# Kernel optimization log

Measured on AMD Instinct MI355X. Metric: run time of the kernel, lower is better.

## Reference

```python
import jax, jax.numpy as jnp
import numpy as np

B, C, H, W = 8, 256, 48, 48
HW = H * W
DK = C // 8
LN_EPS = 1e-5


def setup_inputs() -> dict:
    key = jax.random.key(0)
    ks = jax.random.split(key, 16)
    s = lambda fan: 1.0 / np.sqrt(fan)
    return {
        "img_feat": jax.random.normal(ks[0], (B, C, H, W), jnp.float32),
        "text_feat": jax.random.normal(ks[1], (B, C), jnp.float32),
        "l": jax.random.normal(ks[2], (1, HW), jnp.float32),
        "Wg1": jax.random.normal(ks[3], (C, 2 * C), jnp.float32) * s(C),
        "bg1": jax.random.normal(ks[4], (2 * C,), jnp.float32) * 0.01,
        "ln_g": jnp.ones((2 * C,), jnp.float32),
        "ln_b": jnp.zeros((2 * C,), jnp.float32),
        "Wg2": jax.random.normal(ks[5], (2 * C, C), jnp.float32) * s(2 * C),
        "bg2": jax.random.normal(ks[6], (C,), jnp.float32) * 0.01,
        "Wq": jax.random.normal(ks[7], (DK, C), jnp.float32) * s(C),
        "bq": jax.random.normal(ks[8], (DK,), jnp.float32) * 0.01,
        "Wk": jax.random.normal(ks[9], (DK, C), jnp.float32) * s(C),
        "bk": jax.random.normal(ks[10], (DK,), jnp.float32) * 0.01,
        "Wv": jax.random.normal(ks[11], (C, C), jnp.float32) * s(C),
        "bv": jax.random.normal(ks[12], (C,), jnp.float32) * 0.01,
        "gamma": jax.random.normal(ks[13], (1,), jnp.float32) * 0.1,
    }


def reference(img_feat, text_feat, l, Wg1, bg1, ln_g, ln_b, Wg2, bg2,
              Wq, bq, Wk, bk, Wv, bv, gamma):
    b, c, h, w = img_feat.shape
    hw = h * w
    # G(text_feat): Linear -> LayerNorm -> GELU (exact) -> Linear
    t = text_feat @ Wg1 + bg1                          # [B, 2C]
    mu = jnp.mean(t, axis=-1, keepdims=True)
    var = jnp.mean((t - mu) ** 2, axis=-1, keepdims=True)
    t = (t - mu) / jnp.sqrt(var + LN_EPS) * ln_g + ln_b
    t = jax.nn.gelu(t, approximate=False)
    GvT = t @ Wg2 + bg2                                # [B, C]
    # F_T = GvT^T outer l  -> [B, C, HW]
    FT = GvT[:, :, None] * l.reshape(-1)[None, None, :]
    x = img_feat.reshape(b, c, hw)
    # 1x1 convs are channel matmuls
    Q = jnp.einsum('dc,bcn->bdn', Wq, x) + bq[None, :, None]   # [B, dk, HW]
    K = jnp.einsum('dc,bcn->bdn', Wk, FT) + bk[None, :, None]  # [B, dk, HW]
    V = jnp.einsum('dc,bcn->bdn', Wv, FT) + bv[None, :, None]  # [B, C, HW]
    # energy = Q^T K (NO 1/sqrt(d_k) scaling, as in the source)
    energy = jnp.einsum('bdi,bdj->bij', Q, K)                  # [B, HW, HW]
    attn = jax.nn.softmax(energy, axis=-1)
    out = jnp.einsum('bcj,bij->bci', V, attn).reshape(b, c, h, w)
    return img_feat + gamma.reshape(()) * out
```

## Files before the change

kernel.cpp:

```cpp
#include <hip/hip_runtime.h>
#include <math.h>

#define B_ 8
#define C_ 256
#define C2_ 512
#define DK_ 32
#define HW_ 2304

#define WS_WQ   0
#define WS_VG   2048
#define WS_QB   4096
#define WS_S    4352

__device__ __forceinline__ float gelu_exact(float x) {
    return 0.5f * x * (1.0f + erff(x * 0.70710678118654752f));
}

__global__ __launch_bounds__(512) void k_prep(
    const float* __restrict__ text,
    const float* __restrict__ Wg1,  const float* __restrict__ bg1,
    const float* __restrict__ ln_g, const float* __restrict__ ln_b,
    const float* __restrict__ Wg2,  const float* __restrict__ bg2,
    const float* __restrict__ Wq,   const float* __restrict__ bq,
    const float* __restrict__ Wk,   const float* __restrict__ Wv,
    float* __restrict__ ws)
{
    const int b = blockIdx.x >> 3;
    const int tile = blockIdx.x & 7;
    const int tid = threadIdx.x;

    __shared__ float tx[C_];
    __shared__ __align__(16) float tsh[C2_];
    __shared__ __align__(16) float gvs[C_];
    __shared__ float part2[2][C_];
    __shared__ float r1[8], r2[8];
    __shared__ float kg[DK_];

    if (tid < C_) tx[tid] = text[b * C_ + tid];
    __syncthreads();

    float acc = bg1[tid];
    #pragma unroll 8
    for (int c = 0; c < C_; ++c)
        acc += tx[c] * Wg1[(size_t)c * C2_ + tid];

    float s1 = acc, s2 = acc * acc;
    for (int o = 32; o; o >>= 1) {
        s1 += __shfl_down(s1, o);
        s2 += __shfl_down(s2, o);
    }
    if ((tid & 63) == 0) { r1[tid >> 6] = s1; r2[tid >> 6] = s2; }
    __syncthreads();
    s1 = 0.f; s2 = 0.f;
    #pragma unroll
    for (int u = 0; u < 8; ++u) { s1 += r1[u]; s2 += r2[u]; }
    const float mu = s1 * (1.0f / 512.0f);
    const float rstd = rsqrtf(s2 * (1.0f / 512.0f) - mu * mu + 1e-5f);
    tsh[tid] = gelu_exact((acc - mu) * rstd * ln_g[tid] + ln_b[tid]);
    __syncthreads();

    {
        const int col = tid & 255, half = tid >> 8;
        float g = 0.f;
        const float* wcol = Wg2 + (size_t)(half * 256) * C_ + col;
        #pragma unroll 8
        for (int j = 0; j < 256; ++j)
            g += tsh[half * 256 + j] * wcol[(size_t)j * C_];
        part2[half][col] = g;
    }
    __syncthreads();
    if (tid < C_) gvs[tid] = part2[0][tid] + part2[1][tid] + bg2[tid];
    __syncthreads();

    const int o = tid >> 4, sub = tid & 15;
    const float4* gv4 = (const float4*)gvs + sub * 4;
    {
        const float4* wrow = (const float4*)(Wv + (size_t)(tile * 32 + o) * C_) + sub * 4;
        float a = 0.f;
        #pragma unroll
        for (int k4 = 0; k4 < 4; ++k4) {
            float4 w4 = wrow[k4], g4 = gv4[k4];
            a += w4.x * g4.x + w4.y * g4.y + w4.z * g4.z + w4.w * g4.w;
        }
        a += __shfl_xor(a, 1);
        a += __shfl_xor(a, 2);
        a += __shfl_xor(a, 4);
        a += __shfl_xor(a, 8);
        if (sub == 0) ws[WS_VG + b * C_ + tile * 32 + o] = a;
    }

    if (tile == 0) {
        const float4* wrow = (const float4*)(Wk + (size_t)o * C_) + sub * 4;
        float a = 0.f;
        #pragma unroll
        for (int k4 = 0; k4 < 4; ++k4) {
            float4 w4 = wrow[k4], g4 = gv4[k4];
            a += w4.x * g4.x + w4.y * g4.y + w4.z * g4.z + w4.w * g4.w;
        }
        a += __shfl_xor(a, 1);
        a += __shfl_xor(a, 2);
        a += __shfl_xor(a, 4);
        a += __shfl_xor(a, 8);
        if (sub == 0) kg[o] = a;
        __syncthreads();
        if (tid < C_) {
            float w = 0.f;
            #pragma unroll
            for (int d = 0; d < DK_; ++d) w += kg[d] * Wq[(size_t)d * C_ + tid];
            ws[WS_WQ + b * C_ + tid] = w;
        }
        if (tid == 0) {
            float q = 0.f;
            #pragma unroll
            for (int d = 0; d < DK_; ++d) q += kg[d] * bq[d];
            ws[WS_QB + b] = q;
        }
    }
}

__global__ __launch_bounds__(256) void k_as(
    const float* __restrict__ img, const float* __restrict__ l,
    float* __restrict__ ws)
{
    const int blk = blockIdx.x;
    const int b = blk / 72;
    const int i0 = (blk % 72) * 32;
    const int tid = threadIdx.x;

    __shared__ float lsh[HW_];
    __shared__ float wq[C_];
    __shared__ float part[8][32];
    __shared__ float aa[32];
    __shared__ float redmn[4], redmx[4];

    wq[tid] = ws[WS_WQ + b * C_ + tid];
    float mn = 1e30f, mx = -1e30f;
    #pragma unroll
    for (int j = tid; j < HW_; j += 256) {
        float v = l[j];
        lsh[j] = v;
        mn = fminf(mn, v); mx = fmaxf(mx, v);
    }
    for (int o = 32; o; o >>= 1) {
        mn = fminf(mn, __shfl_down(mn, o));
        mx = fmaxf(mx, __shfl_down(mx, o));
    }
    if ((tid & 63) == 0) { redmn[tid >> 6] = mn; redmx[tid >> 6] = mx; }
    __syncthreads();
    const float lmin = fminf(fminf(redmn[0], redmn[1]), fminf(redmn[2], redmn[3]));
    const float lmax = fmaxf(fmaxf(redmx[0], redmx[1]), fmaxf(redmx[2], redmx[3]));

    {
        const int pix = tid & 31, sub = tid >> 5;
        const float* x = img + ((size_t)b * C_ + sub * 32) * HW_ + i0 + pix;
        float acc = 0.f;
        #pragma unroll 8
        for (int k = 0; k < 32; ++k)
            acc += wq[sub * 32 + k] * x[(size_t)k * HW_];
        part[sub][pix] = acc;
    }
    __syncthreads();
    if (tid < 32) {
        float a = ws[WS_QB + b];
        #pragma unroll
        for (int u = 0; u < 8; ++u) a += part[u][tid];
        aa[tid] = a;
    }
    __syncthreads();

    const int spix = tid >> 3, ssub = tid & 7;
    const float m = aa[spix];
    const float mxv = (m >= 0.f) ? m * lmax : m * lmin;
    float se = 0.f, sle = 0.f;
    #pragma unroll 4
    for (int j = ssub; j < HW_; j += 8) {
        float lj = lsh[j];
        float e = __expf(m * lj - mxv);
        se += e;
        sle += e * lj;
    }
    se += __shfl_xor(se, 1);  sle += __shfl_xor(sle, 1);
    se += __shfl_xor(se, 2);  sle += __shfl_xor(sle, 2);
    se += __shfl_xor(se, 4);  sle += __shfl_xor(sle, 4);
    if (ssub == 0) ws[WS_S + b * HW_ + i0 + spix] = sle / se;
}

__global__ __launch_bounds__(256) void k_out(
    const float* __restrict__ img, const float* __restrict__ bv,
    const float* __restrict__ gamma, const float* __restrict__ ws,
    float* __restrict__ out)
{
    const float g = gamma[0];
    const size_t idx = (size_t)blockIdx.x * 256 + threadIdx.x;
    const size_t flat = idx * 4;
    const int b = (int)(flat / (C_ * HW_));
    const int rem = (int)(flat % (C_ * HW_));
    const int c = rem / HW_;
    const int i = rem % HW_;

    const float4 im = *(const float4*)(img + flat);
    const float4 s4 = *(const float4*)(ws + WS_S + b * HW_ + i);
    const float vgc = ws[WS_VG + b * C_ + c];
    const float bvc = bv[c];
    float4 o;
    o.x = im.x + g * (vgc * s4.x + bvc);
    o.y = im.y + g * (vgc * s4.y + bvc);
    o.z = im.z + g * (vgc * s4.z + bvc);
    o.w = im.w + g * (vgc * s4.w + bvc);
    *(float4*)(out + flat) = o;
}

extern "C" void kernel_launch(void* const* d_in, const int* in_sizes, int n_in,
                              void* d_out, int out_size, void* d_ws, size_t ws_size,
                              hipStream_t stream) {
    const float* img   = (const float*)d_in[0];
    const float* text  = (const float*)d_in[1];
    const float* l     = (const float*)d_in[2];
    const float* Wg1   = (const float*)d_in[3];
    const float* bg1   = (const float*)d_in[4];
    const float* ln_g  = (const float*)d_in[5];
    const float* ln_b  = (const float*)d_in[6];
    const float* Wg2   = (const float*)d_in[7];
    const float* bg2   = (const float*)d_in[8];
    const float* Wq    = (const float*)d_in[9];
    const float* bq    = (const float*)d_in[10];
    const float* Wk    = (const float*)d_in[11];
    const float* Wv    = (const float*)d_in[13];
    const float* bv    = (const float*)d_in[14];
    const float* gamma = (const float*)d_in[15];
    float* out = (float*)d_out;
    float* ws  = (float*)d_ws;

    k_prep<<<64, 512, 0, stream>>>(text, Wg1, bg1, ln_g, ln_b, Wg2, bg2,
                                   Wq, bq, Wk, Wv, ws);
    k_as<<<576, 256, 0, stream>>>(img, l, ws);
    k_out<<<(size_t)B_ * C_ * HW_ / 4 / 256, 256, 0, stream>>>(img, bv, gamma, ws, out);
}
```

Measured before the change: 56.82 us.

## Fuse softmax-stat and output kernels, caching image tile in shared memory

Merges the attention-statistic kernel and the elementwise output kernel into one. Each block keeps its 256x32 image tile in LDS while computing the query projection, then writes the residual output directly from that tile. This removes a second full read of the image, the workspace round trip for the per-pixel statistic, and one kernel launch. In exchange it uses much more LDS per block, which lowers occupancy, and issues narrower scalar stores.

```diff
diff --git a/kernel.cpp b/kernel.cpp
--- a/kernel.cpp
+++ b/kernel.cpp
@@ -10,7 +10,6 @@
 #define WS_WQ   0
 #define WS_VG   2048
 #define WS_QB   4096
-#define WS_S    4352
 
 __device__ __forceinline__ float gelu_exact(float x) {
     return 0.5f * x * (1.0f + erff(x * 0.70710678118654752f));
@@ -118,9 +117,10 @@
     }
 }
 
-__global__ __launch_bounds__(256) void k_as(
+__global__ __launch_bounds__(256) void k_fused(
     const float* __restrict__ img, const float* __restrict__ l,
-    float* __restrict__ ws)
+    const float* __restrict__ bv,  const float* __restrict__ gamma,
+    const float* __restrict__ ws,  float* __restrict__ out)
 {
     const int blk = blockIdx.x;
     const int b = blk / 72;
@@ -128,12 +128,15 @@
     const int tid = threadIdx.x;
 
     __shared__ float lsh[HW_];
-    __shared__ float wq[C_];
+    __shared__ float tile[C_][32];
+    __shared__ float wq[C_], vgb[C_], bvs[C_];
     __shared__ float part[8][32];
-    __shared__ float aa[32];
+    __shared__ float aa[32], ss[32];
     __shared__ float redmn[4], redmx[4];
 
-    wq[tid] = ws[WS_WQ + b * C_ + tid];
+    wq[tid]  = ws[WS_WQ + b * C_ + tid];
+    vgb[tid] = ws[WS_VG + b * C_ + tid];
+    bvs[tid] = bv[tid];
     float mn = 1e30f, mx = -1e30f;
     #pragma unroll
     for (int j = tid; j < HW_; j += 256) {
@@ -150,13 +153,16 @@
     const float lmin = fminf(fminf(redmn[0], redmn[1]), fminf(redmn[2], redmn[3]));
     const float lmax = fmaxf(fmaxf(redmx[0], redmx[1]), fmaxf(redmx[2], redmx[3]));
 
-    {
-        const int pix = tid & 31, sub = tid >> 5;
+    const int pix = tid & 31, sub = tid >> 5;
+    {
         const float* x = img + ((size_t)b * C_ + sub * 32) * HW_ + i0 + pix;
         float acc = 0.f;
         #pragma unroll 8
-        for (int k = 0; k < 32; ++k)
-            acc += wq[sub * 32 + k] * x[(size_t)k * HW_];
+        for (int k = 0; k < 32; ++k) {
+            float v = x[(size_t)k * HW_];
+            tile[sub * 32 + k][pix] = v;
+            acc += wq[sub * 32 + k] * v;
+        }
         part[sub][pix] = acc;
     }
     __syncthreads();
@@ -168,46 +174,35 @@
     }
     __syncthreads();
 
-    const int spix = tid >> 3, ssub = tid & 7;
-    const float m = aa[spix];
-    const float mxv = (m >= 0.f) ? m * lmax : m * lmin;
-    float se = 0.f, sle = 0.f;
-    #pragma unroll 4
-    for (int j = ssub; j < HW_; j += 8) {
-        float lj = lsh[j];
-        float e = __expf(m * lj - mxv);
-        se += e;
-        sle += e * lj;
-    }
-    se += __shfl_xor(se, 1);  sle += __shfl_xor(sle, 1);
-    se += __shfl_xor(se, 2);  sle += __shfl_xor(sle, 2);
-    se += __shfl_xor(se, 4);  sle += __shfl_xor(sle, 4);
-    if (ssub == 0) ws[WS_S + b * HW_ + i0 + spix] = sle / se;
-}
-
-__global__ __launch_bounds__(256) void k_out(
-    const float* __restrict__ img, const float* __restrict__ bv,
-    const float* __restrict__ gamma, const float* __restrict__ ws,
-    float* __restrict__ out)
-{
-    const float g = gamma[0];
-    const size_t idx = (size_t)blockIdx.x * 256 + threadIdx.x;
-    const size_t flat = idx * 4;
-    const int b = (int)(flat / (C_ * HW_));
-    const int rem = (int)(flat % (C_ * HW_));
-    const int c = rem / HW_;
-    const int i = rem % HW_;
-
-    const float4 im = *(const float4*)(img + flat);
-    const float4 s4 = *(const float4*)(ws + WS_S + b * HW_ + i);
-    const float vgc = ws[WS_VG + b * C_ + c];
-    const float bvc = bv[c];
-    float4 o;
-    o.x = im.x + g * (vgc * s4.x + bvc);
-    o.y = im.y + g * (vgc * s4.y + bvc);
-    o.z = im.z + g * (vgc * s4.z + bvc);
-    o.w = im.w + g * (vgc * s4.w + bvc);
-    *(float4*)(out + flat) = o;
+    {
+        const int spix = tid >> 3, ssub = tid & 7;
+        const float m = aa[spix];
+        const float mxv = (m >= 0.f) ? m * lmax : m * lmin;
+        float se = 0.f, sle = 0.f;
+        #pragma unroll 4
+        for (int j = ssub; j < HW_; j += 8) {
+            float lj = lsh[j];
+            float e = __expf(m * lj - mxv);
+            se += e;
+            sle += e * lj;
+        }
+        se += __shfl_xor(se, 1);  sle += __shfl_xor(sle, 1);
+        se += __shfl_xor(se, 2);  sle += __shfl_xor(sle, 2);
+        se += __shfl_xor(se, 4);  sle += __shfl_xor(sle, 4);
+        if (ssub == 0) ss[spix] = sle / se;
+    }
+    __syncthreads();
+
+    {
+        const float g = gamma[0];
+        const float s = ss[pix];
+        float* o = out + ((size_t)b * C_ + sub * 32) * HW_ + i0 + pix;
+        #pragma unroll 8
+        for (int k = 0; k < 32; ++k) {
+            const int c = sub * 32 + k;
+            o[(size_t)k * HW_] = tile[c][pix] + g * (vgb[c] * s + bvs[c]);
+        }
+    }
 }
 
 extern "C" void kernel_launch(void* const* d_in, const int* in_sizes, int n_in,
@@ -233,6 +228,5 @@
 
     k_prep<<<64, 512, 0, stream>>>(text, Wg1, bg1, ln_g, ln_b, Wg2, bg2,
                                    Wq, bq, Wk, Wv, ws);
-    k_as<<<576, 256, 0, stream>>>(img, l, ws);
-    k_out<<<(size_t)B_ * C_ * HW_ / 4 / 256, 256, 0, stream>>>(img, bv, gamma, ws, out);
-}
+    k_fused<<<576, 256, 0, stream>>>(img, l, bv, gamma, ws, out);
+}
```

After: 52.47 us. 7.7% less time.
